# Optimization experiments

Measured on AMD Instinct MI355X. Metric: run time of the kernel, lower is better.

The kernel has to match this reference:

```python
import jax, jax.numpy as jnp
import numpy as np

ALPHA = 1.702  # sigmoid slope in clamped-GLU
LIMIT = 7.0    # clamp limit on gate/up

B, S, H, D, E, K = 2, 2048, 1024, 1024, 8, 2


def setup_inputs() -> dict:
    key = jax.random.key(0)
    ks = jax.random.split(key, 7)
    hidden_states = jax.random.normal(ks[0], (B, S, H), jnp.float32)
    router_indices = jax.random.randint(ks[1], (B * S, K), 0, E)
    routing_weights = jax.random.uniform(ks[2], (B * S, E), dtype=jnp.float32)
    gate_up_proj = jax.random.normal(ks[3], (E, H, 2 * D), jnp.float32) * 0.02
    gate_up_bias = jax.random.normal(ks[4], (E, 2 * D), jnp.float32) * 0.02
    down_proj = jax.random.normal(ks[5], (E, D, H), jnp.float32) * 0.02
    down_bias = jax.random.normal(ks[6], (E, H), jnp.float32) * 0.02
    return dict(hidden_states=hidden_states, router_indices=router_indices,
                routing_weights=routing_weights, gate_up_proj=gate_up_proj,
                gate_up_bias=gate_up_bias, down_proj=down_proj, down_bias=down_bias)


def reference(hidden_states, router_indices, routing_weights,
              gate_up_proj, gate_up_bias, down_proj, down_bias):
    batch = hidden_states.shape[0]
    hs = hidden_states.shape[-1]
    flat = hidden_states.reshape(-1, hs)  # [T, H]
    n_exp = routing_weights.shape[1]
    # index_add with possibly duplicated (token, expert) assignments == count multiplier
    counts = (router_indices[:, :, None] == jnp.arange(n_exp)[None, None, :]).sum(1)  # [T, E]
    w = routing_weights * counts.astype(flat.dtype)  # [T, E] effective combine weight

    def step(out, xs):
        wgu, bgu, wd, bd, we = xs  # wgu:[H,2D] bgu:[2D] wd:[D,H] bd:[H] we:[T]
        gu = flat @ wgu + bgu                      # [T, 2D]
        gate = jnp.minimum(gu[:, ::2], LIMIT)      # interleaved gate channels
        up = jnp.clip(gu[:, 1::2], -LIMIT, LIMIT)  # interleaved up channels
        mid = (up + 1.0) * gate * jax.nn.sigmoid(gate * ALPHA)
        y = mid @ wd + bd                          # [T, H]
        return out + y * we[:, None], None

    out0 = jnp.zeros_like(flat)
    out, _ = jax.lax.scan(step, out0, (gate_up_proj, gate_up_bias, down_proj, down_bias, w.T))
    return out.reshape(batch, -1, hs)
```

## Files before the change

kernel.cpp:

```cpp
#include <hip/hip_runtime.h>
#include <hip/hip_bf16.h>

#define AS1 __attribute__((address_space(1)))
#define AS3 __attribute__((address_space(3)))

typedef __bf16 bf16_8 __attribute__((ext_vector_type(8)));
typedef float f32x4 __attribute__((ext_vector_type(4)));

constexpr int Tn = 4096;
constexpr int Hn = 1024;
constexpr int Dn = 1024;
constexpr int En = 8;
constexpr int Pmax = 10240;
constexpr int MaxT256 = 40;
constexpr float kAlpha = 1.702f;
constexpr float kLimit = 7.0f;

__device__ __forceinline__ unsigned short f2bf(float x) {
  unsigned u = __builtin_bit_cast(unsigned, x);
  u = u + 0x7FFFu + ((u >> 16) & 1u);
  return (unsigned short)(u >> 16);
}
__device__ __forceinline__ unsigned pack2(float a, float b) {
  return (unsigned)f2bf(a) | ((unsigned)f2bf(b) << 16);
}
__device__ __forceinline__ float bflo(unsigned v) { return __builtin_bit_cast(float, v << 16); }
__device__ __forceinline__ float bfhi(unsigned v) { return __builtin_bit_cast(float, v & 0xFFFF0000u); }

__device__ __forceinline__ void gload_lds16(const void* gp, void* lp) {
  __builtin_amdgcn_global_load_lds(
      (const AS1 unsigned int*)(unsigned long long)gp,
      (AS3 unsigned int*)(unsigned int)(unsigned long long)lp,
      16, 0, 0);
}

constexpr int NB_CVT = 4096, NB_TGU = 4096, NB_TDN = 4096;
constexpr int NG1 = MaxT256 * 32;

__global__ void k_prepass(const float* __restrict__ hs, const int* __restrict__ ridx,
                          const float* __restrict__ gup,
                          unsigned short* __restrict__ xb,
                          unsigned short* __restrict__ wg, unsigned short* __restrict__ wu,
                          int* __restrict__ tix, int* __restrict__ pos,
                          int* __restrict__ tileE, int* __restrict__ tileP0,
                          int* __restrict__ ntiles) {
  __shared__ __align__(16) char smem[2 * 32 * 65 * 4 + 64];
  const int tid = threadIdx.x;
  int b = blockIdx.x;

  if (b == 0) {
    int (*lh)[8] = (int(*)[8])smem;
    int* eoff = (int*)(smem + 8192);
#pragma unroll
    for (int e = 0; e < 8; e++) lh[tid][e] = 0;
    int myE[32];
#pragma unroll
    for (int s = 0; s < 32; s++) {
      int e = ridx[tid * 32 + s];
      myE[s] = e;
      lh[tid][e]++;
    }
    __syncthreads();
    if (tid < 8) {
      int tot = 0;
#pragma unroll 1
      for (int t = 0; t < 256; t++) { int v = lh[t][tid]; lh[t][tid] = tot; tot += v; }
      eoff[tid] = tot;
    }
    __syncthreads();
    if (tid == 0) {
      int off = 0, nt = 0;
#pragma unroll 1
      for (int e = 0; e < 8; e++) {
        int cnt = eoff[e];
        eoff[e] = off;
        int ntT = (cnt + 255) >> 8;
        for (int k = 0; k < ntT; k++) { tileE[nt] = e; tileP0[nt] = off + k * 256; nt++; }
        off += ntT * 256;
      }
      *ntiles = nt;
    }
    __syncthreads();
    for (int p = tid; p < Pmax; p += 256) tix[p] = 0;
    __syncthreads();
#pragma unroll
    for (int s = 0; s < 32; s++) {
      int slot = tid * 32 + s;
      int e = myE[s];
      int p = eoff[e] + (lh[tid][e]++);
      pos[slot] = p;
      tix[p] = slot >> 1;
    }
    return;
  }
  b -= 1;

  if (b < NB_CVT) {
    int i = b * 256 + tid;
    float4 v = reinterpret_cast<const float4*>(hs)[i];
    ushort4 o;
    o.x = f2bf(v.x); o.y = f2bf(v.y); o.z = f2bf(v.z); o.w = f2bf(v.w);
    reinterpret_cast<ushort4*>(xb)[i] = o;
    return;
  }
  b -= NB_CVT;

  {
    float (*lg)[65] = (float(*)[65])smem;
    float (*lu)[65] = (float(*)[65])(smem + 32 * 65 * 4);
    const int d0 = (b & 31) * 32, h0 = ((b >> 5) & 15) * 64, e = b >> 9;
    {
      const int hrow = tid >> 2, q = tid & 3;
      const float* src = gup + ((size_t)e * Hn + h0 + hrow) * (2 * Dn) + d0 * 2 + q * 16;
#pragma unroll
      for (int j = 0; j < 4; j++) {
        float4 v = *reinterpret_cast<const float4*>(src + j * 4);
        int dp = q * 8 + j * 2;
        lg[dp][hrow] = v.x; lu[dp][hrow] = v.y;
        lg[dp + 1][hrow] = v.z; lu[dp + 1][hrow] = v.w;
      }
    }
    __syncthreads();
    {
      const int d = tid >> 3, hc = (tid & 7) * 8;
      uint4 og, ou;
      og.x = pack2(lg[d][hc + 0], lg[d][hc + 1]); ou.x = pack2(lu[d][hc + 0], lu[d][hc + 1]);
      og.y = pack2(lg[d][hc + 2], lg[d][hc + 3]); ou.y = pack2(lu[d][hc + 2], lu[d][hc + 3]);
      og.z = pack2(lg[d][hc + 4], lg[d][hc + 5]); ou.z = pack2(lu[d][hc + 4], lu[d][hc + 5]);
      og.w = pack2(lg[d][hc + 6], lg[d][hc + 7]); ou.w = pack2(lu[d][hc + 6], lu[d][hc + 7]);
      *reinterpret_cast<uint4*>(wg + ((size_t)e * Dn + d0 + d) * Hn + h0 + hc) = og;
      *reinterpret_cast<uint4*>(wu + ((size_t)e * Dn + d0 + d) * Hn + h0 + hc) = ou;
    }
  }
}

__launch_bounds__(256, 3)
__global__ void k_main1(const unsigned short* __restrict__ xb,
                        const unsigned short* __restrict__ wg,
                        const unsigned short* __restrict__ wu,
                        const float* __restrict__ gub,
                        const int* __restrict__ tix,
                        const int* __restrict__ tileE,
                        const int* __restrict__ tileP0,
                        const int* __restrict__ ntiles,
                        unsigned short* __restrict__ midc,
                        const float* __restrict__ dwn,
                        unsigned short* __restrict__ wdt) {
  __shared__ __align__(16) char smem[40960];
  const int tid = threadIdx.x;

  if ((int)blockIdx.x >= NG1) {
    int b = blockIdx.x - NG1;
    float (*lt)[65] = (float(*)[65])smem;
    const int h0 = (b & 31) * 32, d0 = ((b >> 5) & 15) * 64, e = b >> 9;
    {
      const int drow = tid >> 2, q = tid & 3;
      const float* src = dwn + ((size_t)e * Dn + d0 + drow) * Hn + h0 + q * 8;
#pragma unroll
      for (int j = 0; j < 2; j++) {
        float4 v = *reinterpret_cast<const float4*>(src + j * 4);
        int hr = q * 8 + j * 4;
        lt[hr][drow] = v.x; lt[hr + 1][drow] = v.y; lt[hr + 2][drow] = v.z; lt[hr + 3][drow] = v.w;
      }
    }
    __syncthreads();
    {
      const int h = tid >> 3, dc = (tid & 7) * 8;
      uint4 o;
      o.x = pack2(lt[h][dc + 0], lt[h][dc + 1]);
      o.y = pack2(lt[h][dc + 2], lt[h][dc + 3]);
      o.z = pack2(lt[h][dc + 4], lt[h][dc + 5]);
      o.w = pack2(lt[h][dc + 6], lt[h][dc + 7]);
      *reinterpret_cast<uint4*>(wdt + ((size_t)e * Hn + h0 + h) * Dn + d0 + dc) = o;
    }
    return;
  }

  unsigned short* Xs = (unsigned short*)smem;
  unsigned short* Bs = (unsigned short*)(smem + 32768);
  const int orig = blockIdx.x;
  const int wgid = (orig & 7) * (NG1 >> 3) + (orig >> 3);
  const int by = wgid & 31;
  const int bx = wgid >> 5;
  if (bx >= *ntiles) return;
  const int e = tileE[bx];
  const int p0 = tileP0[bx];
  const int n0 = by * 32;
  const int wv = tid >> 6, lane = tid & 63;
  const int r8 = lane >> 3, c8 = lane & 7;
  const int fr = lane & 15, kg = lane >> 4;

  int tokc[8];
#pragma unroll
  for (int c = 0; c < 8; c++) tokc[c] = tix[p0 + (c * 4 + wv) * 8 + r8];

  const unsigned short* Gp = wg + ((size_t)e * Dn + n0) * Hn;
  const unsigned short* Up = wu + ((size_t)e * Dn + n0) * Hn;

  f32x4 acc[4][4];
#pragma unroll
  for (int i = 0; i < 4; i++)
#pragma unroll
    for (int j = 0; j < 4; j++) acc[i][j] = f32x4{0.f, 0.f, 0.f, 0.f};

  for (int k0 = 0; k0 < Hn; k0 += 64) {
#pragma unroll
    for (int c = 0; c < 8; c++) {
      int ch = c * 4 + wv;
      gload_lds16(xb + (size_t)tokc[c] * Hn + k0 + c8 * 8, (void*)(Xs + ch * 512));
    }
    {
      gload_lds16(Gp + (size_t)(wv * 8 + r8) * Hn + k0 + c8 * 8, (void*)(Bs + wv * 512));
      gload_lds16(Up + (size_t)(wv * 8 + r8) * Hn + k0 + c8 * 8, (void*)(Bs + (wv + 4) * 512));
    }
    asm volatile("s_waitcnt vmcnt(0)" ::: "memory");
    __syncthreads();
#pragma unroll
    for (int kk = 0; kk < 2; kk++) {
      bf16_8 a[4], b[4];
#pragma unroll
      for (int i = 0; i < 4; i++)
        a[i] = *reinterpret_cast<const bf16_8*>(Xs + (wv * 64 + i * 16 + fr) * 64 + kk * 32 + kg * 8);
#pragma unroll
      for (int j = 0; j < 4; j++)
        b[j] = *reinterpret_cast<const bf16_8*>(Bs + (j * 16 + fr) * 64 + kk * 32 + kg * 8);
#pragma unroll
      for (int i = 0; i < 4; i++)
#pragma unroll
        for (int j = 0; j < 4; j++)
          acc[i][j] = __builtin_amdgcn_mfma_f32_16x16x32_bf16(a[i], b[j], acc[i][j], 0, 0, 0);
    }
    __syncthreads();
  }

  const int rg = kg;
  const float* gb = gub + e * 2 * Dn;
  const int d0 = n0 + fr, d1 = n0 + 16 + fr;
  const float gb0 = gb[2 * d0], ub0 = gb[2 * d0 + 1];
  const float gb1 = gb[2 * d1], ub1 = gb[2 * d1 + 1];
#pragma unroll
  for (int i = 0; i < 4; i++) {
#pragma unroll
    for (int r = 0; r < 4; r++) {
      int row = p0 + wv * 64 + i * 16 + rg * 4 + r;
      {
        float g = acc[i][0][r] + gb0;
        float u = acc[i][2][r] + ub0;
        g = fminf(g, kLimit);
        u = fminf(fmaxf(u, -kLimit), kLimit);
        float sg = 1.0f / (1.0f + __expf(-kAlpha * g));
        midc[(size_t)row * Dn + d0] = f2bf((u + 1.0f) * g * sg);
      }
      {
        float g = acc[i][1][r] + gb1;
        float u = acc[i][3][r] + ub1;
        g = fminf(g, kLimit);
        u = fminf(fmaxf(u, -kLimit), kLimit);
        float sg = 1.0f / (1.0f + __expf(-kAlpha * g));
        midc[(size_t)row * Dn + d1] = f2bf((u + 1.0f) * g * sg);
      }
    }
  }
}

__launch_bounds__(256, 3)
__global__ void k_gemm2(const unsigned short* __restrict__ midc,
                        const unsigned short* __restrict__ wdt,
                        const int* __restrict__ tileE,
                        const int* __restrict__ tileP0,
                        const int* __restrict__ ntiles,
                        unsigned short* __restrict__ ys) {
  __shared__ __align__(16) unsigned short As[256 * 64];
  __shared__ __align__(16) unsigned short Bs[64 * 64];
  const int nwg = gridDim.x;
  const int orig = blockIdx.x;
  const int wgid = (orig & 7) * (nwg >> 3) + (orig >> 3);
  const int by = wgid & 15;
  const int bx = wgid >> 4;
  if (bx >= *ntiles) return;
  const int e = tileE[bx];
  const int p0 = tileP0[bx];
  const int n0 = by * 64;
  const int tid = threadIdx.x;
  const int wv = tid >> 6, lane = tid & 63;
  const int r8 = lane >> 3, c8 = lane & 7;
  const int fr = lane & 15, kg = lane >> 4;
  const unsigned short* Ap = midc + (size_t)p0 * Dn;
  const unsigned short* Bp = wdt + ((size_t)e * Hn + n0) * Dn;

  f32x4 acc[4][4];
#pragma unroll
  for (int i = 0; i < 4; i++)
#pragma unroll
    for (int j = 0; j < 4; j++) acc[i][j] = f32x4{0.f, 0.f, 0.f, 0.f};

  for (int k0 = 0; k0 < Dn; k0 += 64) {
#pragma unroll
    for (int c = 0; c < 8; c++) {
      int ch = c * 4 + wv;
      gload_lds16(Ap + (size_t)(ch * 8 + r8) * Dn + k0 + c8 * 8, (void*)(As + ch * 512));
    }
#pragma unroll
    for (int c = 0; c < 2; c++) {
      int ch = c * 4 + wv;
      gload_lds16(Bp + (size_t)(ch * 8 + r8) * Dn + k0 + c8 * 8, (void*)(Bs + ch * 512));
    }
    asm volatile("s_waitcnt vmcnt(0)" ::: "memory");
    __syncthreads();
#pragma unroll
    for (int kk = 0; kk < 2; kk++) {
      bf16_8 a[4], b[4];
#pragma unroll
      for (int i = 0; i < 4; i++)
        a[i] = *reinterpret_cast<const bf16_8*>(As + (wv * 64 + i * 16 + fr) * 64 + kk * 32 + kg * 8);
#pragma unroll
      for (int j = 0; j < 4; j++)
        b[j] = *reinterpret_cast<const bf16_8*>(Bs + (j * 16 + fr) * 64 + kk * 32 + kg * 8);
#pragma unroll
      for (int i = 0; i < 4; i++)
#pragma unroll
        for (int j = 0; j < 4; j++)
          acc[i][j] = __builtin_amdgcn_mfma_f32_16x16x32_bf16(a[i], b[j], acc[i][j], 0, 0, 0);
    }
    __syncthreads();
  }

  const int rg = kg;
#pragma unroll
  for (int i = 0; i < 4; i++)
#pragma unroll
    for (int r = 0; r < 4; r++) {
      int row = p0 + wv * 64 + i * 16 + rg * 4 + r;
#pragma unroll
      for (int j = 0; j < 4; j++) {
        int col = n0 + j * 16 + fr;
        ys[(size_t)row * Hn + col] = f2bf(acc[i][j][r]);
      }
    }
}

__global__ void k_combine(const unsigned short* __restrict__ ys, const int* __restrict__ ridx,
                          const float* __restrict__ rw, const int* __restrict__ pos,
                          const float* __restrict__ db, float* __restrict__ out) {
  int idx = blockIdx.x * blockDim.x + threadIdx.x;
  int t = idx >> 7, hc = (idx & 127) << 3;
  int e0 = ridx[2 * t], e1 = ridx[2 * t + 1];
  int p0 = pos[2 * t], p1 = pos[2 * t + 1];
  float w0 = rw[t * En + e0], w1 = rw[t * En + e1];
  uint4 ya = *reinterpret_cast<const uint4*>(ys + (size_t)p0 * Hn + hc);
  uint4 yb = *reinterpret_cast<const uint4*>(ys + (size_t)p1 * Hn + hc);
  float4 da0 = *reinterpret_cast<const float4*>(db + (size_t)e0 * Hn + hc);
  float4 da1 = *reinterpret_cast<const float4*>(db + (size_t)e0 * Hn + hc + 4);
  float4 db0 = *reinterpret_cast<const float4*>(db + (size_t)e1 * Hn + hc);
  float4 db1 = *reinterpret_cast<const float4*>(db + (size_t)e1 * Hn + hc + 4);
  float4 o0, o1;
  o0.x = w0 * (bflo(ya.x) + da0.x) + w1 * (bflo(yb.x) + db0.x);
  o0.y = w0 * (bfhi(ya.x) + da0.y) + w1 * (bfhi(yb.x) + db0.y);
  o0.z = w0 * (bflo(ya.y) + da0.z) + w1 * (bflo(yb.y) + db0.z);
  o0.w = w0 * (bfhi(ya.y) + da0.w) + w1 * (bfhi(yb.y) + db0.w);
  o1.x = w0 * (bflo(ya.z) + da1.x) + w1 * (bflo(yb.z) + db1.x);
  o1.y = w0 * (bfhi(ya.z) + da1.y) + w1 * (bfhi(yb.z) + db1.y);
  o1.z = w0 * (bflo(ya.w) + da1.z) + w1 * (bflo(yb.w) + db1.z);
  o1.w = w0 * (bfhi(ya.w) + da1.w) + w1 * (bfhi(yb.w) + db1.w);
  *reinterpret_cast<float4*>(out + (size_t)t * Hn + hc) = o0;
  *reinterpret_cast<float4*>(out + (size_t)t * Hn + hc + 4) = o1;
}

extern "C" void kernel_launch(void* const* d_in, const int* in_sizes, int n_in,
                              void* d_out, int out_size, void* d_ws, size_t ws_size,
                              hipStream_t stream) {
  (void)in_sizes; (void)n_in; (void)out_size; (void)ws_size;
  const float* hs  = (const float*)d_in[0];
  const int*   ri  = (const int*)d_in[1];
  const float* rw  = (const float*)d_in[2];
  const float* gup = (const float*)d_in[3];
  const float* gub = (const float*)d_in[4];
  const float* dwn = (const float*)d_in[5];
  const float* db  = (const float*)d_in[6];
  float* out = (float*)d_out;

  char* ws = (char*)d_ws;
  int* tix    = (int*)(ws);
  int* pos    = (int*)(ws + 65536);
  int* tileE  = (int*)(ws + 131072);
  int* tileP0 = (int*)(ws + 131584);
  int* ntiles = (int*)(ws + 132096);
  unsigned short* xb   = (unsigned short*)(ws + 262144);
  unsigned short* wg   = (unsigned short*)(ws + 262144 + 8388608);
  unsigned short* wu   = (unsigned short*)(ws + 262144 + 8388608 + 16777216);
  unsigned short* wdt  = (unsigned short*)(ws + 262144 + 8388608 + 2*16777216);
  unsigned short* midc = (unsigned short*)(ws + 262144 + 8388608 + 3*16777216);
  unsigned short* ys   = (unsigned short*)(ws + 262144 + 8388608 + 3*16777216 + (size_t)Pmax * Dn * 2);

  k_prepass<<<dim3(1 + NB_CVT + NB_TGU), dim3(256), 0, stream>>>(
      hs, ri, gup, xb, wg, wu, tix, pos, tileE, tileP0, ntiles);
  k_main1<<<dim3(NG1 + NB_TDN), dim3(256), 0, stream>>>(
      xb, wg, wu, gub, tix, tileE, tileP0, ntiles, midc, dwn, wdt);
  k_gemm2<<<dim3(MaxT256 * 16), dim3(256), 0, stream>>>(
      midc, wdt, tileE, tileP0, ntiles, ys);
  k_combine<<<dim3(Tn * Hn / 8 / 256), dim3(256), 0, stream>>>(ys, ri, rw, pos, db, out);
}
```

Before: 131.1 us.

## Rewrite gate/up GEMM with 128x256 tiles, triple-buffered LDS and XOR swizzle

Replaces the first grouped GEMM with a 512-thread kernel. Each block computes a 128-token by 128-channel (gate+up) tile and streams K through a three-slot LDS ring with async global-to-LDS loads, partial vmcnt waits, an XOR swizzle against bank conflicts, and raised priority around the MFMA block. The down-projection weight transpose moves from the GEMM1 launch into the prepass, and a second tile list with 128-row tiles is built for the new kernel. This aims to hide load latency behind compute and raise per-block reuse, at the cost of one block per CU, large LDS use and more prepass work.

```diff
diff --git a/kernel.cpp b/kernel.cpp
--- a/kernel.cpp
+++ b/kernel.cpp
@@ -13,6 +13,7 @@
 constexpr int En = 8;
 constexpr int Pmax = 10240;
 constexpr int MaxT256 = 40;
+constexpr int MaxT128 = 80;
 constexpr float kAlpha = 1.702f;
 constexpr float kLimit = 7.0f;
 
@@ -35,15 +36,16 @@
 }
 
 constexpr int NB_CVT = 4096, NB_TGU = 4096, NB_TDN = 4096;
-constexpr int NG1 = MaxT256 * 32;
 
 __global__ void k_prepass(const float* __restrict__ hs, const int* __restrict__ ridx,
-                          const float* __restrict__ gup,
+                          const float* __restrict__ gup, const float* __restrict__ dwn,
                           unsigned short* __restrict__ xb,
                           unsigned short* __restrict__ wg, unsigned short* __restrict__ wu,
+                          unsigned short* __restrict__ wdt,
                           int* __restrict__ tix, int* __restrict__ pos,
                           int* __restrict__ tileE, int* __restrict__ tileP0,
-                          int* __restrict__ ntiles) {
+                          int* __restrict__ tileE2, int* __restrict__ tileP02,
+                          int* __restrict__ ntiles, int* __restrict__ ntiles2) {
   __shared__ __align__(16) char smem[2 * 32 * 65 * 4 + 64];
   const int tid = threadIdx.x;
   int b = blockIdx.x;
@@ -69,16 +71,21 @@
     }
     __syncthreads();
     if (tid == 0) {
-      int off = 0, nt = 0;
+      int off = 0, nt = 0, nt2 = 0;
 #pragma unroll 1
       for (int e = 0; e < 8; e++) {
         int cnt = eoff[e];
         eoff[e] = off;
         int ntT = (cnt + 255) >> 8;
-        for (int k = 0; k < ntT; k++) { tileE[nt] = e; tileP0[nt] = off + k * 256; nt++; }
+        for (int k = 0; k < ntT; k++) {
+          tileE[nt] = e; tileP0[nt] = off + k * 256; nt++;
+          tileE2[nt2] = e; tileP02[nt2] = off + k * 256; nt2++;
+          tileE2[nt2] = e; tileP02[nt2] = off + k * 256 + 128; nt2++;
+        }
         off += ntT * 256;
       }
       *ntiles = nt;
+      *ntiles2 = nt2;
     }
     __syncthreads();
     for (int p = tid; p < Pmax; p += 256) tix[p] = 0;
@@ -105,7 +112,7 @@
   }
   b -= NB_CVT;
 
-  {
+  if (b < NB_TGU) {
     float (*lg)[65] = (float(*)[65])smem;
     float (*lu)[65] = (float(*)[65])(smem + 32 * 65 * 4);
     const int d0 = (b & 31) * 32, h0 = ((b >> 5) & 15) * 64, e = b >> 9;
@@ -131,26 +138,11 @@
       *reinterpret_cast<uint4*>(wg + ((size_t)e * Dn + d0 + d) * Hn + h0 + hc) = og;
       *reinterpret_cast<uint4*>(wu + ((size_t)e * Dn + d0 + d) * Hn + h0 + hc) = ou;
     }
-  }
-}
-
-__launch_bounds__(256, 3)
-__global__ void k_main1(const unsigned short* __restrict__ xb,
-                        const unsigned short* __restrict__ wg,
-                        const unsigned short* __restrict__ wu,
-                        const float* __restrict__ gub,
-                        const int* __restrict__ tix,
-                        const int* __restrict__ tileE,
-                        const int* __restrict__ tileP0,
-                        const int* __restrict__ ntiles,
-                        unsigned short* __restrict__ midc,
-                        const float* __restrict__ dwn,
-                        unsigned short* __restrict__ wdt) {
-  __shared__ __align__(16) char smem[40960];
-  const int tid = threadIdx.x;
-
-  if ((int)blockIdx.x >= NG1) {
-    int b = blockIdx.x - NG1;
+    return;
+  }
+  b -= NB_TGU;
+
+  {
     float (*lt)[65] = (float(*)[65])smem;
     const int h0 = (b & 31) * 32, d0 = ((b >> 5) & 15) * 64, e = b >> 9;
     {
@@ -173,91 +165,130 @@
       o.w = pack2(lt[h][dc + 6], lt[h][dc + 7]);
       *reinterpret_cast<uint4*>(wdt + ((size_t)e * Hn + h0 + h) * Dn + d0 + dc) = o;
     }
-    return;
-  }
-
-  unsigned short* Xs = (unsigned short*)smem;
-  unsigned short* Bs = (unsigned short*)(smem + 32768);
+  }
+}
+
+__launch_bounds__(512, 1)
+__global__ void k_gemm1(const unsigned short* __restrict__ xb,
+                        const unsigned short* __restrict__ wg,
+                        const unsigned short* __restrict__ wu,
+                        const float* __restrict__ gub,
+                        const int* __restrict__ tix,
+                        const int* __restrict__ tileE2,
+                        const int* __restrict__ tileP02,
+                        const int* __restrict__ ntiles2,
+                        unsigned short* __restrict__ midc) {
+  __shared__ __align__(16) unsigned short Abuf[3][128 * 64];
+  __shared__ __align__(16) unsigned short Bbuf[3][256 * 64];
+
+  const int nwg = gridDim.x;
   const int orig = blockIdx.x;
-  const int wgid = (orig & 7) * (NG1 >> 3) + (orig >> 3);
-  const int by = wgid & 31;
-  const int bx = wgid >> 5;
-  if (bx >= *ntiles) return;
-  const int e = tileE[bx];
-  const int p0 = tileP0[bx];
-  const int n0 = by * 32;
+  const int wgid = (orig & 7) * (nwg >> 3) + (orig >> 3);
+  const int bx = wgid >> 3;
+  const int panel = wgid & 7;
+  if (bx >= *ntiles2) return;
+  const int e = tileE2[bx];
+  const int p0 = tileP02[bx];
+  const int n0 = panel * 128;
+
+  const int tid = threadIdx.x;
   const int wv = tid >> 6, lane = tid & 63;
-  const int r8 = lane >> 3, c8 = lane & 7;
+  const int wr = wv >> 2, wc = wv & 3;
+  const int l8 = lane >> 3;
   const int fr = lane & 15, kg = lane >> 4;
-
-  int tokc[8];
-#pragma unroll
-  for (int c = 0; c < 8; c++) tokc[c] = tix[p0 + (c * 4 + wv) * 8 + r8];
+  const int c8s = (lane & 7) ^ (((lane >> 5) & 1) << 1);
+  const int xorv = (lane & 4) << 3;
+
+  int tokc[2];
+#pragma unroll
+  for (int c = 0; c < 2; c++) tokc[c] = tix[p0 + (c * 8 + wv) * 8 + l8];
 
   const unsigned short* Gp = wg + ((size_t)e * Dn + n0) * Hn;
   const unsigned short* Up = wu + ((size_t)e * Dn + n0) * Hn;
 
+  auto stage = [&](int kt, int slot) {
+    const int k0 = kt * 64;
+    unsigned short* Ad = Abuf[slot];
+    unsigned short* Bd = Bbuf[slot];
+#pragma unroll
+    for (int c = 0; c < 2; c++) {
+      int ch = c * 8 + wv;
+      gload_lds16(xb + (size_t)tokc[c] * Hn + k0 + c8s * 8, (void*)(Ad + ch * 512));
+    }
+#pragma unroll
+    for (int c = 0; c < 4; c++) {
+      int ch = c * 8 + wv;
+      const unsigned short* src = (ch & 2) ? Up : Gp;
+      int drow = (ch >> 2) * 16 + (ch & 1) * 8 + l8;
+      gload_lds16(src + (size_t)drow * Hn + k0 + c8s * 8, (void*)(Bd + ch * 512));
+    }
+  };
+
   f32x4 acc[4][4];
 #pragma unroll
   for (int i = 0; i < 4; i++)
 #pragma unroll
     for (int j = 0; j < 4; j++) acc[i][j] = f32x4{0.f, 0.f, 0.f, 0.f};
 
-  for (int k0 = 0; k0 < Hn; k0 += 64) {
-#pragma unroll
-    for (int c = 0; c < 8; c++) {
-      int ch = c * 4 + wv;
-      gload_lds16(xb + (size_t)tokc[c] * Hn + k0 + c8 * 8, (void*)(Xs + ch * 512));
-    }
-    {
-      gload_lds16(Gp + (size_t)(wv * 8 + r8) * Hn + k0 + c8 * 8, (void*)(Bs + wv * 512));
-      gload_lds16(Up + (size_t)(wv * 8 + r8) * Hn + k0 + c8 * 8, (void*)(Bs + (wv + 4) * 512));
-    }
-    asm volatile("s_waitcnt vmcnt(0)" ::: "memory");
-    __syncthreads();
+  stage(0, 0);
+  stage(1, 1);
+  asm volatile("s_waitcnt vmcnt(6)" ::: "memory");
+  __builtin_amdgcn_s_barrier();
+
+  constexpr int NSTEP = 16;
+  for (int t = 0; t < NSTEP; ++t) {
+    if (t + 2 < NSTEP) stage(t + 2, (t + 2) % 3);
+    const char* Ab = (const char*)Abuf[t % 3];
+    const char* Bb = (const char*)Bbuf[t % 3];
 #pragma unroll
     for (int kk = 0; kk < 2; kk++) {
       bf16_8 a[4], b[4];
 #pragma unroll
       for (int i = 0; i < 4; i++)
-        a[i] = *reinterpret_cast<const bf16_8*>(Xs + (wv * 64 + i * 16 + fr) * 64 + kk * 32 + kg * 8);
+        a[i] = *reinterpret_cast<const bf16_8*>(
+            Ab + (((wr * 64 + i * 16 + fr) * 128 + kk * 64 + kg * 16) ^ xorv));
 #pragma unroll
       for (int j = 0; j < 4; j++)
-        b[j] = *reinterpret_cast<const bf16_8*>(Bs + (j * 16 + fr) * 64 + kk * 32 + kg * 8);
+        b[j] = *reinterpret_cast<const bf16_8*>(
+            Bb + (((wc * 64 + j * 16 + fr) * 128 + kk * 64 + kg * 16) ^ xorv));
+      __builtin_amdgcn_s_setprio(1);
 #pragma unroll
       for (int i = 0; i < 4; i++)
 #pragma unroll
         for (int j = 0; j < 4; j++)
           acc[i][j] = __builtin_amdgcn_mfma_f32_16x16x32_bf16(a[i], b[j], acc[i][j], 0, 0, 0);
-    }
-    __syncthreads();
+      __builtin_amdgcn_s_setprio(0);
+    }
+    if (t < NSTEP - 2) asm volatile("s_waitcnt vmcnt(6)" ::: "memory");
+    else               asm volatile("s_waitcnt vmcnt(0)" ::: "memory");
+    __builtin_amdgcn_s_barrier();
   }
 
   const int rg = kg;
   const float* gb = gub + e * 2 * Dn;
-  const int d0 = n0 + fr, d1 = n0 + 16 + fr;
-  const float gb0 = gb[2 * d0], ub0 = gb[2 * d0 + 1];
-  const float gb1 = gb[2 * d1], ub1 = gb[2 * d1 + 1];
+  const int dA = n0 + wc * 32 + fr, dB = dA + 16;
+  const float gb0 = gb[2 * dA], ub0 = gb[2 * dA + 1];
+  const float gb1 = gb[2 * dB], ub1 = gb[2 * dB + 1];
 #pragma unroll
   for (int i = 0; i < 4; i++) {
 #pragma unroll
     for (int r = 0; r < 4; r++) {
-      int row = p0 + wv * 64 + i * 16 + rg * 4 + r;
+      int row = p0 + wr * 64 + i * 16 + rg * 4 + r;
       {
         float g = acc[i][0][r] + gb0;
-        float u = acc[i][2][r] + ub0;
+        float u = acc[i][1][r] + ub0;
         g = fminf(g, kLimit);
         u = fminf(fmaxf(u, -kLimit), kLimit);
         float sg = 1.0f / (1.0f + __expf(-kAlpha * g));
-        midc[(size_t)row * Dn + d0] = f2bf((u + 1.0f) * g * sg);
+        midc[(size_t)row * Dn + dA] = f2bf((u + 1.0f) * g * sg);
       }
       {
-        float g = acc[i][1][r] + gb1;
+        float g = acc[i][2][r] + gb1;
         float u = acc[i][3][r] + ub1;
         g = fminf(g, kLimit);
         u = fminf(fmaxf(u, -kLimit), kLimit);
         float sg = 1.0f / (1.0f + __expf(-kAlpha * g));
-        midc[(size_t)row * Dn + d1] = f2bf((u + 1.0f) * g * sg);
+        midc[(size_t)row * Dn + dB] = f2bf((u + 1.0f) * g * sg);
       }
     }
   }
@@ -380,11 +411,14 @@
   float* out = (float*)d_out;
 
   char* ws = (char*)d_ws;
-  int* tix    = (int*)(ws);
-  int* pos    = (int*)(ws + 65536);
-  int* tileE  = (int*)(ws + 131072);
-  int* tileP0 = (int*)(ws + 131584);
-  int* ntiles = (int*)(ws + 132096);
+  int* tix     = (int*)(ws);
+  int* pos     = (int*)(ws + 65536);
+  int* tileE   = (int*)(ws + 131072);
+  int* tileP0  = (int*)(ws + 131584);
+  int* tileE2  = (int*)(ws + 132096);
+  int* tileP02 = (int*)(ws + 132608);
+  int* ntiles  = (int*)(ws + 133120);
+  int* ntiles2 = (int*)(ws + 133124);
   unsigned short* xb   = (unsigned short*)(ws + 262144);
   unsigned short* wg   = (unsigned short*)(ws + 262144 + 8388608);
   unsigned short* wu   = (unsigned short*)(ws + 262144 + 8388608 + 16777216);
@@ -392,10 +426,10 @@
   unsigned short* midc = (unsigned short*)(ws + 262144 + 8388608 + 3*16777216);
   unsigned short* ys   = (unsigned short*)(ws + 262144 + 8388608 + 3*16777216 + (size_t)Pmax * Dn * 2);
 
-  k_prepass<<<dim3(1 + NB_CVT + NB_TGU), dim3(256), 0, stream>>>(
-      hs, ri, gup, xb, wg, wu, tix, pos, tileE, tileP0, ntiles);
-  k_main1<<<dim3(NG1 + NB_TDN), dim3(256), 0, stream>>>(
-      xb, wg, wu, gub, tix, tileE, tileP0, ntiles, midc, dwn, wdt);
+  k_prepass<<<dim3(1 + NB_CVT + NB_TGU + NB_TDN), dim3(256), 0, stream>>>(
+      hs, ri, gup, dwn, xb, wg, wu, wdt, tix, pos, tileE, tileP0, tileE2, tileP02, ntiles, ntiles2);
+  k_gemm1<<<dim3(MaxT128 * 8), dim3(512), 0, stream>>>(
+      xb, wg, wu, gub, tix, tileE2, tileP02, ntiles2, midc);
   k_gemm2<<<dim3(MaxT256 * 16), dim3(256), 0, stream>>>(
       midc, wdt, tileE, tileP0, ntiles, ys);
   k_combine<<<dim3(Tn * Hn / 8 / 256), dim3(256), 0, stream>>>(ys, ri, rw, pos, db, out);
```

New measurement: 137.3 us. +4.7%, slower.

## Pre-gather routed tokens into contiguous bf16 buffer and interleave gate/up weight panels

Applied to the files above, without the earlier changes.

Routing moves into its own single-block kernel. The conversion pass then gathers hidden-state rows by routed slot into a contiguous bf16 buffer, so GEMM1 loads A rows contiguously instead of through per-row token indirection. Gate and up weights are written into one panel-interleaved buffer, so each 64-row B tile is contiguous. This adds a kernel launch, serialises routing before the conversion pass, and writes a larger gathered buffer (Pmax rows instead of T), in exchange for simpler, more coalesced GEMM1 loads.

```diff
diff --git a/kernel.cpp b/kernel.cpp
--- a/kernel.cpp
+++ b/kernel.cpp
@@ -34,81 +34,80 @@
       16, 0, 0);
 }
 
-constexpr int NB_CVT = 4096, NB_TGU = 4096, NB_TDN = 4096;
-constexpr int NG1 = MaxT256 * 32;
-
-__global__ void k_prepass(const float* __restrict__ hs, const int* __restrict__ ridx,
-                          const float* __restrict__ gup,
-                          unsigned short* __restrict__ xb,
-                          unsigned short* __restrict__ wg, unsigned short* __restrict__ wu,
-                          int* __restrict__ tix, int* __restrict__ pos,
-                          int* __restrict__ tileE, int* __restrict__ tileP0,
-                          int* __restrict__ ntiles) {
+__global__ void k_route(const int* __restrict__ ridx,
+                        int* __restrict__ tix, int* __restrict__ pos,
+                        int* __restrict__ tileE, int* __restrict__ tileP0,
+                        int* __restrict__ ntiles) {
+  __shared__ int lh[256][8];
+  __shared__ int eoff[8];
+  const int tid = threadIdx.x;
+#pragma unroll
+  for (int e = 0; e < 8; e++) lh[tid][e] = 0;
+  int myE[32];
+#pragma unroll
+  for (int s = 0; s < 32; s++) {
+    int e = ridx[tid * 32 + s];
+    myE[s] = e;
+    lh[tid][e]++;
+  }
+  __syncthreads();
+  if (tid < 8) {
+    int tot = 0;
+#pragma unroll 1
+    for (int t = 0; t < 256; t++) { int v = lh[t][tid]; lh[t][tid] = tot; tot += v; }
+    eoff[tid] = tot;
+  }
+  __syncthreads();
+  if (tid == 0) {
+    int off = 0, nt = 0;
+#pragma unroll 1
+    for (int e = 0; e < 8; e++) {
+      int cnt = eoff[e];
+      eoff[e] = off;
+      int ntT = (cnt + 255) >> 8;
+      for (int k = 0; k < ntT; k++) { tileE[nt] = e; tileP0[nt] = off + k * 256; nt++; }
+      off += ntT * 256;
+    }
+    *ntiles = nt;
+  }
+  __syncthreads();
+  for (int p = tid; p < Pmax; p += 256) tix[p] = 0;
+  __syncthreads();
+#pragma unroll
+  for (int s = 0; s < 32; s++) {
+    int slot = tid * 32 + s;
+    int e = myE[s];
+    int p = eoff[e] + (lh[tid][e]++);
+    pos[slot] = p;
+    tix[p] = slot >> 1;
+  }
+}
+
+constexpr int NB_TGU = 4096, NB_TDN = 4096;
+constexpr int NGEMM1 = MaxT256 * 32;
+
+__global__ void k_prep(const float* __restrict__ hs, const int* __restrict__ tix,
+                       const float* __restrict__ gup,
+                       unsigned short* __restrict__ xg, unsigned short* __restrict__ wgu) {
   __shared__ __align__(16) char smem[2 * 32 * 65 * 4 + 64];
   const int tid = threadIdx.x;
   int b = blockIdx.x;
 
-  if (b == 0) {
-    int (*lh)[8] = (int(*)[8])smem;
-    int* eoff = (int*)(smem + 8192);
-#pragma unroll
-    for (int e = 0; e < 8; e++) lh[tid][e] = 0;
-    int myE[32];
-#pragma unroll
-    for (int s = 0; s < 32; s++) {
-      int e = ridx[tid * 32 + s];
-      myE[s] = e;
-      lh[tid][e]++;
-    }
-    __syncthreads();
-    if (tid < 8) {
-      int tot = 0;
-#pragma unroll 1
-      for (int t = 0; t < 256; t++) { int v = lh[t][tid]; lh[t][tid] = tot; tot += v; }
-      eoff[tid] = tot;
-    }
-    __syncthreads();
-    if (tid == 0) {
-      int off = 0, nt = 0;
-#pragma unroll 1
-      for (int e = 0; e < 8; e++) {
-        int cnt = eoff[e];
-        eoff[e] = off;
-        int ntT = (cnt + 255) >> 8;
-        for (int k = 0; k < ntT; k++) { tileE[nt] = e; tileP0[nt] = off + k * 256; nt++; }
-        off += ntT * 256;
-      }
-      *ntiles = nt;
-    }
-    __syncthreads();
-    for (int p = tid; p < Pmax; p += 256) tix[p] = 0;
-    __syncthreads();
-#pragma unroll
-    for (int s = 0; s < 32; s++) {
-      int slot = tid * 32 + s;
-      int e = myE[s];
-      int p = eoff[e] + (lh[tid][e]++);
-      pos[slot] = p;
-      tix[p] = slot >> 1;
-    }
-    return;
-  }
-  b -= 1;
-
-  if (b < NB_CVT) {
-    int i = b * 256 + tid;
-    float4 v = reinterpret_cast<const float4*>(hs)[i];
+  if (b < Pmax) {
+    const int t = tix[b];
+    float4 v = *reinterpret_cast<const float4*>(hs + (size_t)t * Hn + tid * 4);
     ushort4 o;
     o.x = f2bf(v.x); o.y = f2bf(v.y); o.z = f2bf(v.z); o.w = f2bf(v.w);
-    reinterpret_cast<ushort4*>(xb)[i] = o;
+    *reinterpret_cast<ushort4*>(xg + (size_t)b * Hn + tid * 4) = o;
     return;
   }
-  b -= NB_CVT;
+  b -= Pmax;
 
   {
     float (*lg)[65] = (float(*)[65])smem;
     float (*lu)[65] = (float(*)[65])(smem + 32 * 65 * 4);
-    const int d0 = (b & 31) * 32, h0 = ((b >> 5) & 15) * 64, e = b >> 9;
+    const int g0 = b & 31;
+    const int d0 = g0 * 32, h0 = ((b >> 5) & 15) * 64, e = b >> 9;
     {
       const int hrow = tid >> 2, q = tid & 3;
       const float* src = gup + ((size_t)e * Hn + h0 + hrow) * (2 * Dn) + d0 * 2 + q * 16;
@@ -128,18 +127,17 @@
       og.y = pack2(lg[d][hc + 2], lg[d][hc + 3]); ou.y = pack2(lu[d][hc + 2], lu[d][hc + 3]);
       og.z = pack2(lg[d][hc + 4], lg[d][hc + 5]); ou.z = pack2(lu[d][hc + 4], lu[d][hc + 5]);
       og.w = pack2(lg[d][hc + 6], lg[d][hc + 7]); ou.w = pack2(lu[d][hc + 6], lu[d][hc + 7]);
-      *reinterpret_cast<uint4*>(wg + ((size_t)e * Dn + d0 + d) * Hn + h0 + hc) = og;
-      *reinterpret_cast<uint4*>(wu + ((size_t)e * Dn + d0 + d) * Hn + h0 + hc) = ou;
+      unsigned short* base = wgu + (((size_t)e * 32 + g0) * 64) * Hn + h0 + hc;
+      *reinterpret_cast<uint4*>(base + (size_t)d * Hn) = og;
+      *reinterpret_cast<uint4*>(base + (size_t)(32 + d) * Hn) = ou;
     }
   }
 }
 
 __launch_bounds__(256, 3)
-__global__ void k_main1(const unsigned short* __restrict__ xb,
-                        const unsigned short* __restrict__ wg,
-                        const unsigned short* __restrict__ wu,
+__global__ void k_main1(const unsigned short* __restrict__ xg,
+                        const unsigned short* __restrict__ wgu,
                         const float* __restrict__ gub,
-                        const int* __restrict__ tix,
                         const int* __restrict__ tileE,
                         const int* __restrict__ tileP0,
                         const int* __restrict__ ntiles,
@@ -149,8 +147,8 @@
   __shared__ __align__(16) char smem[40960];
   const int tid = threadIdx.x;
 
-  if ((int)blockIdx.x >= NG1) {
-    int b = blockIdx.x - NG1;
+  if ((int)blockIdx.x >= NGEMM1) {
+    int b = blockIdx.x - NGEMM1;
     float (*lt)[65] = (float(*)[65])smem;
     const int h0 = (b & 31) * 32, d0 = ((b >> 5) & 15) * 64, e = b >> 9;
     {
@@ -176,26 +174,22 @@
     return;
   }
 
-  unsigned short* Xs = (unsigned short*)smem;
+  unsigned short* As = (unsigned short*)smem;
   unsigned short* Bs = (unsigned short*)(smem + 32768);
+  const int nwg = NGEMM1;
   const int orig = blockIdx.x;
-  const int wgid = (orig & 7) * (NG1 >> 3) + (orig >> 3);
-  const int by = wgid & 31;
+  const int wgid = (orig & 7) * (nwg >> 3) + (orig >> 3);
+  const int panel = wgid & 31;
   const int bx = wgid >> 5;
   if (bx >= *ntiles) return;
   const int e = tileE[bx];
   const int p0 = tileP0[bx];
-  const int n0 = by * 32;
+  const int n0 = panel * 32;
   const int wv = tid >> 6, lane = tid & 63;
   const int r8 = lane >> 3, c8 = lane & 7;
   const int fr = lane & 15, kg = lane >> 4;
-
-  int tokc[8];
-#pragma unroll
-  for (int c = 0; c < 8; c++) tokc[c] = tix[p0 + (c * 4 + wv) * 8 + r8];
-
-  const unsigned short* Gp = wg + ((size_t)e * Dn + n0) * Hn;
-  const unsigned short* Up = wu + ((size_t)e * Dn + n0) * Hn;
+  const unsigned short* Ap = xg + (size_t)p0 * Hn;
+  const unsigned short* Bp = wgu + (((size_t)e * 32 + panel) * 64) * Hn;
 
   f32x4 acc[4][4];
 #pragma unroll
@@ -207,11 +201,12 @@
 #pragma unroll
     for (int c = 0; c < 8; c++) {
       int ch = c * 4 + wv;
-      gload_lds16(xb + (size_t)tokc[c] * Hn + k0 + c8 * 8, (void*)(Xs + ch * 512));
-    }
-    {
-      gload_lds16(Gp + (size_t)(wv * 8 + r8) * Hn + k0 + c8 * 8, (void*)(Bs + wv * 512));
-      gload_lds16(Up + (size_t)(wv * 8 + r8) * Hn + k0 + c8 * 8, (void*)(Bs + (wv + 4) * 512));
+      gload_lds16(Ap + (size_t)(ch * 8 + r8) * Hn + k0 + c8 * 8, (void*)(As + ch * 512));
+    }
+#pragma unroll
+    for (int c = 0; c < 2; c++) {
+      int ch = c * 4 + wv;
+      gload_lds16(Bp + (size_t)(ch * 8 + r8) * Hn + k0 + c8 * 8, (void*)(Bs + ch * 512));
     }
     asm volatile("s_waitcnt vmcnt(0)" ::: "memory");
     __syncthreads();
@@ -220,7 +215,7 @@
       bf16_8 a[4], b[4];
 #pragma unroll
       for (int i = 0; i < 4; i++)
-        a[i] = *reinterpret_cast<const bf16_8*>(Xs + (wv * 64 + i * 16 + fr) * 64 + kk * 32 + kg * 8);
+        a[i] = *reinterpret_cast<const bf16_8*>(As + (wv * 64 + i * 16 + fr) * 64 + kk * 32 + kg * 8);
 #pragma unroll
       for (int j = 0; j < 4; j++)
         b[j] = *reinterpret_cast<const bf16_8*>(Bs + (j * 16 + fr) * 64 + kk * 32 + kg * 8);
@@ -385,17 +380,16 @@
   int* tileE  = (int*)(ws + 131072);
   int* tileP0 = (int*)(ws + 131584);
   int* ntiles = (int*)(ws + 132096);
-  unsigned short* xb   = (unsigned short*)(ws + 262144);
-  unsigned short* wg   = (unsigned short*)(ws + 262144 + 8388608);
-  unsigned short* wu   = (unsigned short*)(ws + 262144 + 8388608 + 16777216);
-  unsigned short* wdt  = (unsigned short*)(ws + 262144 + 8388608 + 2*16777216);
-  unsigned short* midc = (unsigned short*)(ws + 262144 + 8388608 + 3*16777216);
-  unsigned short* ys   = (unsigned short*)(ws + 262144 + 8388608 + 3*16777216 + (size_t)Pmax * Dn * 2);
-
-  k_prepass<<<dim3(1 + NB_CVT + NB_TGU), dim3(256), 0, stream>>>(
-      hs, ri, gup, xb, wg, wu, tix, pos, tileE, tileP0, ntiles);
-  k_main1<<<dim3(NG1 + NB_TDN), dim3(256), 0, stream>>>(
-      xb, wg, wu, gub, tix, tileE, tileP0, ntiles, midc, dwn, wdt);
+  unsigned short* xg   = (unsigned short*)(ws + 262144);
+  unsigned short* wgu  = (unsigned short*)(ws + 262144 + 20971520);
+  unsigned short* wdt  = (unsigned short*)(ws + 262144 + 20971520 + 33554432);
+  unsigned short* midc = (unsigned short*)(ws + 262144 + 20971520 + 33554432 + 16777216);
+  unsigned short* ys   = (unsigned short*)(ws + 262144 + 20971520 + 33554432 + 16777216 + 20971520);
+
+  k_route<<<dim3(1), dim3(256), 0, stream>>>(ri, tix, pos, tileE, tileP0, ntiles);
+  k_prep<<<dim3(Pmax + NB_TGU), dim3(256), 0, stream>>>(hs, tix, gup, xg, wgu);
+  k_main1<<<dim3(NGEMM1 + NB_TDN), dim3(256), 0, stream>>>(
+      xg, wgu, gub, tileE, tileP0, ntiles, midc, dwn, wdt);
   k_gemm2<<<dim3(MaxT256 * 16), dim3(256), 0, stream>>>(
       midc, wdt, tileE, tileP0, ntiles, ys);
   k_combine<<<dim3(Tn * Hn / 8 / 256), dim3(256), 0, stream>>>(ys, ri, rw, pos, db, out);
```

Result: slower. 150.6 us (+14.8%).

## Widen GEMM1 tile to 128 columns with 512-thread blocks and interleaved gate/up panels

Applied to the files above, without the earlier changes.

The first GEMM moves from a 256x32-output tile (gate and up halves) on 256 threads to a 256x64-output tile on 512 threads arranged as a 4x2 wave grid. Gate and up weights are stored interleaved in 32-row groups in one buffer so each block loads one contiguous 128-row B panel. This halves the number of times each token row is gathered into LDS per expert, cutting A-side traffic. The down-projection transpose blocks are also resized to 64x64 tiles with 512 threads. The trade-off is more registers and LDS per block, which may reduce occupancy.

```diff
diff --git a/kernel.cpp b/kernel.cpp
--- a/kernel.cpp
+++ b/kernel.cpp
@@ -34,13 +34,13 @@
       16, 0, 0);
 }
 
-constexpr int NB_CVT = 4096, NB_TGU = 4096, NB_TDN = 4096;
-constexpr int NG1 = MaxT256 * 32;
+constexpr int NB_CVT = 4096, NB_TGU = 4096;
+constexpr int NGEMM1 = MaxT256 * 16;
+constexpr int NB_TDN = 2048;
 
 __global__ void k_prepass(const float* __restrict__ hs, const int* __restrict__ ridx,
                           const float* __restrict__ gup,
-                          unsigned short* __restrict__ xb,
-                          unsigned short* __restrict__ wg, unsigned short* __restrict__ wu,
+                          unsigned short* __restrict__ xb, unsigned short* __restrict__ wgu,
                           int* __restrict__ tix, int* __restrict__ pos,
                           int* __restrict__ tileE, int* __restrict__ tileP0,
                           int* __restrict__ ntiles) {
@@ -108,7 +108,8 @@
   {
     float (*lg)[65] = (float(*)[65])smem;
     float (*lu)[65] = (float(*)[65])(smem + 32 * 65 * 4);
-    const int d0 = (b & 31) * 32, h0 = ((b >> 5) & 15) * 64, e = b >> 9;
+    const int g0 = b & 31;
+    const int d0 = g0 * 32, h0 = ((b >> 5) & 15) * 64, e = b >> 9;
     {
       const int hrow = tid >> 2, q = tid & 3;
       const float* src = gup + ((size_t)e * Hn + h0 + hrow) * (2 * Dn) + d0 * 2 + q * 16;
@@ -128,16 +129,16 @@
       og.y = pack2(lg[d][hc + 2], lg[d][hc + 3]); ou.y = pack2(lu[d][hc + 2], lu[d][hc + 3]);
       og.z = pack2(lg[d][hc + 4], lg[d][hc + 5]); ou.z = pack2(lu[d][hc + 4], lu[d][hc + 5]);
       og.w = pack2(lg[d][hc + 6], lg[d][hc + 7]); ou.w = pack2(lu[d][hc + 6], lu[d][hc + 7]);
-      *reinterpret_cast<uint4*>(wg + ((size_t)e * Dn + d0 + d) * Hn + h0 + hc) = og;
-      *reinterpret_cast<uint4*>(wu + ((size_t)e * Dn + d0 + d) * Hn + h0 + hc) = ou;
-    }
-  }
-}
-
-__launch_bounds__(256, 3)
+      unsigned short* base = wgu + (((size_t)e * 32 + g0) * 64) * Hn + h0 + hc;
+      *reinterpret_cast<uint4*>(base + (size_t)d * Hn) = og;
+      *reinterpret_cast<uint4*>(base + (size_t)(32 + d) * Hn) = ou;
+    }
+  }
+}
+
+__launch_bounds__(512, 4)
 __global__ void k_main1(const unsigned short* __restrict__ xb,
-                        const unsigned short* __restrict__ wg,
-                        const unsigned short* __restrict__ wu,
+                        const unsigned short* __restrict__ wgu,
                         const float* __restrict__ gub,
                         const int* __restrict__ tix,
                         const int* __restrict__ tileE,
@@ -146,22 +147,21 @@
                         unsigned short* __restrict__ midc,
                         const float* __restrict__ dwn,
                         unsigned short* __restrict__ wdt) {
-  __shared__ __align__(16) char smem[40960];
+  __shared__ __align__(16) char smem[49152];
   const int tid = threadIdx.x;
 
-  if ((int)blockIdx.x >= NG1) {
-    int b = blockIdx.x - NG1;
+  if ((int)blockIdx.x >= NGEMM1) {
+    int b = blockIdx.x - NGEMM1;
     float (*lt)[65] = (float(*)[65])smem;
-    const int h0 = (b & 31) * 32, d0 = ((b >> 5) & 15) * 64, e = b >> 9;
+    const int h0 = (b & 15) * 64, d0 = ((b >> 4) & 15) * 64, e = b >> 8;
     {
-      const int drow = tid >> 2, q = tid & 3;
+      const int drow = tid >> 3, q = tid & 7;
       const float* src = dwn + ((size_t)e * Dn + d0 + drow) * Hn + h0 + q * 8;
-#pragma unroll
-      for (int j = 0; j < 2; j++) {
-        float4 v = *reinterpret_cast<const float4*>(src + j * 4);
-        int hr = q * 8 + j * 4;
-        lt[hr][drow] = v.x; lt[hr + 1][drow] = v.y; lt[hr + 2][drow] = v.z; lt[hr + 3][drow] = v.w;
-      }
+      float4 v0 = *reinterpret_cast<const float4*>(src);
+      float4 v1 = *reinterpret_cast<const float4*>(src + 4);
+      int hr = q * 8;
+      lt[hr + 0][drow] = v0.x; lt[hr + 1][drow] = v0.y; lt[hr + 2][drow] = v0.z; lt[hr + 3][drow] = v0.w;
+      lt[hr + 4][drow] = v1.x; lt[hr + 5][drow] = v1.y; lt[hr + 6][drow] = v1.z; lt[hr + 7][drow] = v1.w;
     }
     __syncthreads();
     {
@@ -176,26 +176,26 @@
     return;
   }
 
-  unsigned short* Xs = (unsigned short*)smem;
+  unsigned short* As = (unsigned short*)smem;
   unsigned short* Bs = (unsigned short*)(smem + 32768);
+  const int nwg = NGEMM1;
   const int orig = blockIdx.x;
-  const int wgid = (orig & 7) * (NG1 >> 3) + (orig >> 3);
-  const int by = wgid & 31;
-  const int bx = wgid >> 5;
+  const int wgid = (orig & 7) * (nwg >> 3) + (orig >> 3);
+  const int panel = wgid & 15;
+  const int bx = wgid >> 4;
   if (bx >= *ntiles) return;
   const int e = tileE[bx];
   const int p0 = tileP0[bx];
-  const int n0 = by * 32;
   const int wv = tid >> 6, lane = tid & 63;
-  const int r8 = lane >> 3, c8 = lane & 7;
+  const int wr = wv >> 1, wc = wv & 1;
+  const int l8 = lane >> 3, c8 = lane & 7;
   const int fr = lane & 15, kg = lane >> 4;
 
-  int tokc[8];
-#pragma unroll
-  for (int c = 0; c < 8; c++) tokc[c] = tix[p0 + (c * 4 + wv) * 8 + r8];
-
-  const unsigned short* Gp = wg + ((size_t)e * Dn + n0) * Hn;
-  const unsigned short* Up = wu + ((size_t)e * Dn + n0) * Hn;
+  int tokc[4];
+#pragma unroll
+  for (int c = 0; c < 4; c++) tokc[c] = tix[p0 + (c * 8 + wv) * 8 + l8];
+
+  const unsigned short* Bp = wgu + (((size_t)e * 32 + panel * 2) * 64) * Hn;
 
   f32x4 acc[4][4];
 #pragma unroll
@@ -205,13 +205,14 @@
 
   for (int k0 = 0; k0 < Hn; k0 += 64) {
 #pragma unroll
-    for (int c = 0; c < 8; c++) {
-      int ch = c * 4 + wv;
-      gload_lds16(xb + (size_t)tokc[c] * Hn + k0 + c8 * 8, (void*)(Xs + ch * 512));
-    }
-    {
-      gload_lds16(Gp + (size_t)(wv * 8 + r8) * Hn + k0 + c8 * 8, (void*)(Bs + wv * 512));
-      gload_lds16(Up + (size_t)(wv * 8 + r8) * Hn + k0 + c8 * 8, (void*)(Bs + (wv + 4) * 512));
+    for (int c = 0; c < 4; c++) {
+      int ch = c * 8 + wv;
+      gload_lds16(xb + (size_t)tokc[c] * Hn + k0 + c8 * 8, (void*)(As + ch * 512));
+    }
+#pragma unroll
+    for (int c = 0; c < 2; c++) {
+      int ch = c * 8 + wv;
+      gload_lds16(Bp + (size_t)(ch * 8 + l8) * Hn + k0 + c8 * 8, (void*)(Bs + ch * 512));
     }
     asm volatile("s_waitcnt vmcnt(0)" ::: "memory");
     __syncthreads();
@@ -220,10 +221,10 @@
       bf16_8 a[4], b[4];
 #pragma unroll
       for (int i = 0; i < 4; i++)
-        a[i] = *reinterpret_cast<const bf16_8*>(Xs + (wv * 64 + i * 16 + fr) * 64 + kk * 32 + kg * 8);
+        a[i] = *reinterpret_cast<const bf16_8*>(As + (wr * 64 + i * 16 + fr) * 64 + kk * 32 + kg * 8);
 #pragma unroll
       for (int j = 0; j < 4; j++)
-        b[j] = *reinterpret_cast<const bf16_8*>(Bs + (j * 16 + fr) * 64 + kk * 32 + kg * 8);
+        b[j] = *reinterpret_cast<const bf16_8*>(Bs + (wc * 64 + j * 16 + fr) * 64 + kk * 32 + kg * 8);
 #pragma unroll
       for (int i = 0; i < 4; i++)
 #pragma unroll
@@ -233,23 +234,23 @@
     __syncthreads();
   }
 
-  const int rg = kg;
+  const int G0 = (panel * 2 + wc) * 32;
   const float* gb = gub + e * 2 * Dn;
-  const int d0 = n0 + fr, d1 = n0 + 16 + fr;
-  const float gb0 = gb[2 * d0], ub0 = gb[2 * d0 + 1];
-  const float gb1 = gb[2 * d1], ub1 = gb[2 * d1 + 1];
+  const int d0e = G0 + fr, d1e = G0 + 16 + fr;
+  const float gb0 = gb[2 * d0e], ub0 = gb[2 * d0e + 1];
+  const float gb1 = gb[2 * d1e], ub1 = gb[2 * d1e + 1];
 #pragma unroll
   for (int i = 0; i < 4; i++) {
 #pragma unroll
     for (int r = 0; r < 4; r++) {
-      int row = p0 + wv * 64 + i * 16 + rg * 4 + r;
+      int row = p0 + wr * 64 + i * 16 + kg * 4 + r;
       {
         float g = acc[i][0][r] + gb0;
         float u = acc[i][2][r] + ub0;
         g = fminf(g, kLimit);
         u = fminf(fmaxf(u, -kLimit), kLimit);
         float sg = 1.0f / (1.0f + __expf(-kAlpha * g));
-        midc[(size_t)row * Dn + d0] = f2bf((u + 1.0f) * g * sg);
+        midc[(size_t)row * Dn + d0e] = f2bf((u + 1.0f) * g * sg);
       }
       {
         float g = acc[i][1][r] + gb1;
@@ -257,7 +258,7 @@
         g = fminf(g, kLimit);
         u = fminf(fmaxf(u, -kLimit), kLimit);
         float sg = 1.0f / (1.0f + __expf(-kAlpha * g));
-        midc[(size_t)row * Dn + d1] = f2bf((u + 1.0f) * g * sg);
+        midc[(size_t)row * Dn + d1e] = f2bf((u + 1.0f) * g * sg);
       }
     }
   }
@@ -386,16 +387,15 @@
   int* tileP0 = (int*)(ws + 131584);
   int* ntiles = (int*)(ws + 132096);
   unsigned short* xb   = (unsigned short*)(ws + 262144);
-  unsigned short* wg   = (unsigned short*)(ws + 262144 + 8388608);
-  unsigned short* wu   = (unsigned short*)(ws + 262144 + 8388608 + 16777216);
-  unsigned short* wdt  = (unsigned short*)(ws + 262144 + 8388608 + 2*16777216);
-  unsigned short* midc = (unsigned short*)(ws + 262144 + 8388608 + 3*16777216);
-  unsigned short* ys   = (unsigned short*)(ws + 262144 + 8388608 + 3*16777216 + (size_t)Pmax * Dn * 2);
+  unsigned short* wgu  = (unsigned short*)(ws + 262144 + 8388608);
+  unsigned short* wdt  = (unsigned short*)(ws + 262144 + 8388608 + 33554432);
+  unsigned short* midc = (unsigned short*)(ws + 262144 + 8388608 + 33554432 + 16777216);
+  unsigned short* ys   = (unsigned short*)(ws + 262144 + 8388608 + 33554432 + 16777216 + 20971520);
 
   k_prepass<<<dim3(1 + NB_CVT + NB_TGU), dim3(256), 0, stream>>>(
-      hs, ri, gup, xb, wg, wu, tix, pos, tileE, tileP0, ntiles);
-  k_main1<<<dim3(NG1 + NB_TDN), dim3(256), 0, stream>>>(
-      xb, wg, wu, gub, tix, tileE, tileP0, ntiles, midc, dwn, wdt);
+      hs, ri, gup, xb, wgu, tix, pos, tileE, tileP0, ntiles);
+  k_main1<<<dim3(NGEMM1 + NB_TDN), dim3(512), 0, stream>>>(
+      xb, wgu, gub, tix, tileE, tileP0, ntiles, midc, dwn, wdt);
   k_gemm2<<<dim3(MaxT256 * 16), dim3(256), 0, stream>>>(
       midc, wdt, tileE, tileP0, ntiles, ys);
   k_combine<<<dim3(Tn * Hn / 8 / 256), dim3(256), 0, stream>>>(ys, ri, rw, pos, db, out);
```

After: 151.4 us. 1.15x slower.
